# Optimization experiments

Hardware: AMD Instinct MI355X
Metric: run time of the kernel (lower is better)

Reference implementation:

```python
import jax, jax.numpy as jnp
import numpy as np

B, O, F = 64, 64, 1024
RN, RD = 16, 256
DEPTH = 2


def setup_inputs() -> dict:
    key = jax.random.key(0)
    ks = jax.random.split(key, 7)
    s_self = (2.0 / (F + F)) ** 0.5  # xavier-ish scale
    s_rel = (2.0 / (F + RD + F)) ** 0.5
    return {
        "x": jax.random.normal(ks[0], (B, O, F), jnp.float32),
        "A": jax.random.uniform(ks[1], (B, O, O * RN), jnp.float32),
        "R": jax.random.normal(ks[2], (RN, RD), jnp.float32),
        "Wself": jax.random.normal(ks[3], (DEPTH, F, F), jnp.float32) * s_self,
        "bself": jax.random.normal(ks[4], (DEPTH, F), jnp.float32) * 0.02,
        "Wrel": jax.random.normal(ks[5], (DEPTH, F + RD, F), jnp.float32) * s_rel,
        "brel": jax.random.normal(ks[6], (DEPTH, F), jnp.float32) * 0.02,
    }


def reference(x, A, R, Wself, bself, Wrel, brel):
    # x: [B,O,F], A: [B,O,O*RN], R: [RN,RD]
    b, o, f = x.shape
    rn = R.shape[0]
    depth = Wself.shape[0]
    for i in range(depth):
        # self transform: Linear(F -> F)
        xs = x @ Wself[i] + bself[i]  # [B,O,F]
        # relation transform: Linear(F+RD -> F) applied to concat(x_repeated, R_repeated).
        # Exact decomposition of the concat: first F rows of Wrel act on x, rest on R.
        xr_x = x @ Wrel[i][:f]                 # [B,O,F]
        xr_r = R @ Wrel[i][f:] + brel[i]       # [RN,F]
        xr = (xr_x[:, :, None, :] + xr_r[None, None, :, :]).reshape(b, o * rn, f)
        agg = jnp.matmul(A, xr)                # [B,O,F]
        x = jnp.tanh(xs + agg + x)             # residual + tanh
    return x
```

## Files before the change

### kernel.cpp

```cpp
#include <hip/hip_runtime.h>
#include <hip/hip_bf16.h>
#include <math.h>

#define B 64
#define O 64
#define F 1024
#define RN 16
#define RD 256
#define DEPTH 2
#define M (B*O)

typedef __attribute__((ext_vector_type(8))) _Float16 half8;
typedef __attribute__((ext_vector_type(4))) float f32x4;

#define RES_SCALE 2048.0f
#define RES_INV  (1.0f/2048.0f)

__device__ __forceinline__ unsigned short h2u(_Float16 h) {
  union { _Float16 h; unsigned short u; } c; c.h = h; return c.u;
}
__device__ __forceinline__ void split2(float x, unsigned short& h, unsigned short& l) {
  _Float16 hh = (_Float16)x;
  _Float16 ll = (_Float16)((x - (float)hh) * RES_SCALE);
  h = h2u(hh); l = h2u(ll);
}

__device__ __forceinline__ void gload_lds16(const unsigned short* g, void* l) {
  __builtin_amdgcn_global_load_lds(
      (const __attribute__((address_space(1))) unsigned int*)g,
      (__attribute__((address_space(3))) unsigned int*)l, 16, 0, 0);
}

__global__ __launch_bounds__(256) void k_reduceA(const float* __restrict__ A,
                                                 float* __restrict__ A1,
                                                 float* __restrict__ A2) {
  __shared__ float row[O * RN];
  const int bo = blockIdx.x;
  const int t = threadIdx.x;
  *reinterpret_cast<float4*>(&row[t * 4]) =
      *reinterpret_cast<const float4*>(&A[(size_t)bo * (O * RN) + t * 4]);
  __syncthreads();
  if (t < O) {
    float s = 0.f;
#pragma unroll
    for (int r = 0; r < RN; ++r) s += row[t * RN + r];
    A1[(size_t)bo * O + t] = s;
  } else if (t < O + RN) {
    const int r = t - O;
    float s = 0.f;
#pragma unroll
    for (int o2 = 0; o2 < O; ++o2) s += row[o2 * RN + r];
    A2[(size_t)bo * RN + r] = s;
  }
}

__global__ __launch_bounds__(256) void k_xrr(const float* __restrict__ R,
                                             const float* __restrict__ Wrel,
                                             const float* __restrict__ brel,
                                             float* __restrict__ xrr) {
  const int layer = blockIdx.y;
  const float* Wr = Wrel + (size_t)layer * (F + RD) * F + (size_t)F * F;
  const float* br = brel + (size_t)layer * F;
  const int r = blockIdx.x >> 2;
  const int n = ((blockIdx.x & 3) << 8) + threadIdx.x;
  float s = br[n];
  for (int k = 0; k < RD; ++k) s += R[r * RD + k] * Wr[(size_t)k * F + n];
  xrr[(size_t)layer * RN * F + (size_t)r * F + n] = s;
}

__global__ __launch_bounds__(256) void k_splitX(const float* __restrict__ X,
                                                unsigned short* __restrict__ Xh,
                                                unsigned short* __restrict__ Xl) {
  const size_t i = ((size_t)blockIdx.x * 256 + threadIdx.x) * 4;
  const float4 v = *reinterpret_cast<const float4*>(&X[i]);
  unsigned short h0, h1, h2, h3, l0, l1, l2, l3;
  split2(v.x, h0, l0); split2(v.y, h1, l1); split2(v.z, h2, l2); split2(v.w, h3, l3);
  uint2 hp, lp;
  hp.x = (unsigned)h0 | ((unsigned)h1 << 16); hp.y = (unsigned)h2 | ((unsigned)h3 << 16);
  lp.x = (unsigned)l0 | ((unsigned)l1 << 16); lp.y = (unsigned)l2 | ((unsigned)l3 << 16);
  *reinterpret_cast<uint2*>(&Xh[i]) = hp;
  *reinterpret_cast<uint2*>(&Xl[i]) = lp;
}

__global__ __launch_bounds__(256) void k_splitW2(const float* __restrict__ Wself,
                                                 const float* __restrict__ Wrel,
                                                 unsigned short* __restrict__ Wht,
                                                 unsigned short* __restrict__ Wlt) {
  __shared__ float T[32][33];
  const int layer = blockIdx.z >> 1;
  const int sel = blockIdx.z & 1;
  const float* W = sel ? (Wrel + (size_t)layer * (F + RD) * F)
                       : (Wself + (size_t)layer * F * F);
  const size_t obase = (size_t)layer * 2048 * 1024 + (size_t)(sel ? 1024 : 0) * 1024;
  const int k0 = blockIdx.x * 32, n0 = blockIdx.y * 32;
  const int t = threadIdx.x;
  const int r = t >> 3, c4 = (t & 7) << 2;
  const float4 v = *reinterpret_cast<const float4*>(&W[(size_t)(k0 + r) * 1024 + n0 + c4]);
  T[r][c4] = v.x; T[r][c4 + 1] = v.y; T[r][c4 + 2] = v.z; T[r][c4 + 3] = v.w;
  __syncthreads();
  unsigned short h[4], l[4];
#pragma unroll
  for (int j = 0; j < 4; ++j) split2(T[c4 + j][r], h[j], l[j]);
  uint2 hp, lp;
  hp.x = (unsigned)h[0] | ((unsigned)h[1] << 16); hp.y = (unsigned)h[2] | ((unsigned)h[3] << 16);
  lp.x = (unsigned)l[0] | ((unsigned)l[1] << 16); lp.y = (unsigned)l[2] | ((unsigned)l[3] << 16);
  const size_t o = obase + (size_t)(n0 + r) * 1024 + k0 + c4;
  *reinterpret_cast<uint2*>(&Wht[o]) = hp;
  *reinterpret_cast<uint2*>(&Wlt[o]) = lp;
}

__device__ __forceinline__ void stage_tiles8(const unsigned short* __restrict__ Asrc,
                                             const unsigned short* __restrict__ Bsrc,
                                             int bm, int bn, int k0,
                                             int w, int lane,
                                             char* Al, char* Bl) {
  const int srow = lane >> 3;
  const int sin = (lane & 7) << 4;
#pragma unroll
  for (int i = 0; i < 4; ++i) {
    const int c = (w << 2) + i;
    const int cc = c & 15;
    const int row = (cc << 3) + srow;
    const int inrow = sin ^ ((row & 7) << 4);
    const unsigned short* src = (c < 16) ? Asrc : Bsrc;
    const int rbase = (c < 16) ? bm : bn;
    char* ldst = (c < 16) ? Al : Bl;
    gload_lds16(src + ((size_t)(rbase + row) << 10) + k0 + (inrow >> 1), ldst + (cc << 10));
  }
}

__device__ __forceinline__ void compute_tile8(const char* Al, const char* Bl,
                                              int ar, int br, int kbyte,
                                              f32x4 (&acc)[4][2]) {
#pragma unroll
  for (int kk = 0; kk < 2; ++kk) {
    half8 a[4], b[2];
#pragma unroll
    for (int m = 0; m < 4; ++m) {
      const int row = ar + m * 16;
      const int off = (row << 7) + (((kk << 6) + kbyte) ^ ((row & 7) << 4));
      a[m] = *reinterpret_cast<const half8*>(&Al[off]);
    }
#pragma unroll
    for (int n = 0; n < 2; ++n) {
      const int row = br + n * 16;
      const int off = (row << 7) + (((kk << 6) + kbyte) ^ ((row & 7) << 4));
      b[n] = *reinterpret_cast<const half8*>(&Bl[off]);
    }
#pragma unroll
    for (int m = 0; m < 4; ++m)
#pragma unroll
      for (int n = 0; n < 2; ++n)
        acc[m][n] = __builtin_amdgcn_mfma_f32_16x16x32_f16(a[m], b[n], acc[m][n], 0, 0, 0);
  }
}

__device__ __forceinline__ void gemm_piece8(const unsigned short* __restrict__ Asrc,
                                            const unsigned short* __restrict__ Bsrc,
                                            int bm, int bn, int w, int lane,
                                            int ar, int br, int kbyte,
                                            char* Al, char* Bl, f32x4 (&acc)[4][2]) {
  for (int kt = 0; kt < 16; ++kt) {
    stage_tiles8(Asrc, Bsrc, bm, bn, kt << 6, w, lane, Al, Bl);
    __syncthreads();
    compute_tile8(Al, Bl, ar, br, kbyte, acc);
    __syncthreads();
  }
}

__global__ __launch_bounds__(512) void k_gemm_mfma(
    const unsigned short* __restrict__ Xh, const unsigned short* __restrict__ Xl,
    const unsigned short* __restrict__ Wht, const unsigned short* __restrict__ Wlt,
    float* __restrict__ xs, float* __restrict__ xrx, int xs_full) {
  __shared__ __align__(16) char Al[128 * 128];
  __shared__ __align__(16) char Bl[128 * 128];
  const int t = threadIdx.x;
  const int lane = t & 63, w = t >> 6;
  const int bid = blockIdx.x;
  const int half = bid & 1;
  int e = bid >> 1;
  e = (e & 7) * 32 + (e >> 3);
  const int bm = (e & 31) * 128;
  const int bn = (e >> 5) * 128 + (half ? 0 : 1024);
  const int wr = w >> 2, wc = w & 3;
  const bool full = (half == 0) || xs_full;

  f32x4 accM[4][2], accR[4][2];
#pragma unroll
  for (int m = 0; m < 4; ++m)
#pragma unroll
    for (int n = 0; n < 2; ++n) { accM[m][n] = (f32x4)0.f; accR[m][n] = (f32x4)0.f; }

  const int ar = wr * 64 + (lane & 15);
  const int br = wc * 32 + (lane & 15);
  const int kbyte = (lane >> 4) << 4;

  gemm_piece8(Xh, Wht, bm, bn, w, lane, ar, br, kbyte, Al, Bl, accM);
  if (full) {
    gemm_piece8(Xh, Wlt, bm, bn, w, lane, ar, br, kbyte, Al, Bl, accR);
    gemm_piece8(Xl, Wht, bm, bn, w, lane, ar, br, kbyte, Al, Bl, accR);
  }

  float* dst = (bn < 1024) ? xs : xrx;
  const int coff = bn & 1023;
  const int lrow = (lane >> 4) << 2;
  const int lcol = lane & 15;
#pragma unroll
  for (int m = 0; m < 4; ++m)
#pragma unroll
    for (int n = 0; n < 2; ++n) {
      const int gr = bm + wr * 64 + m * 16 + lrow;
      const int gc = coff + wc * 32 + n * 16 + lcol;
#pragma unroll
      for (int i = 0; i < 4; ++i)
        dst[((size_t)(gr + i) << 10) + gc] = accM[m][n][i] + accR[m][n][i] * RES_INV;
    }
}

__global__ __launch_bounds__(256) void k_agg(const float* __restrict__ A1,
                                             const float* __restrict__ A2,
                                             const float* __restrict__ xrx,
                                             const float* __restrict__ xrr,
                                             const float* __restrict__ xs,
                                             const float* __restrict__ bias,
                                             const float* __restrict__ xin,
                                             float* __restrict__ xout,
                                             unsigned short* __restrict__ XhO,
                                             unsigned short* __restrict__ XlO) {
  __shared__ float A1s[O][O + 1];
  __shared__ float A2s[O][RN + 1];
  __shared__ float Xls[O][132];
  __shared__ float Rls[RN][132];
  const int b = blockIdx.x;
  const int f0 = blockIdx.y * 128;
  const int t = threadIdx.x;

#pragma unroll
  for (int i = 0; i < 4; ++i) {
    const int gi = i * 1024 + t * 4;
    const float4 v = *reinterpret_cast<const float4*>(&A1[(size_t)b * O * O + gi]);
    const int o = gi >> 6, c = gi & 63;
    A1s[o][c] = v.x; A1s[o][c + 1] = v.y; A1s[o][c + 2] = v.z; A1s[o][c + 3] = v.w;
  }
  {
    const int gi = t * 4;
    const float4 v = *reinterpret_cast<const float4*>(&A2[(size_t)b * O * RN + gi]);
    const int o = gi >> 4, c = gi & 15;
    A2s[o][c] = v.x; A2s[o][c + 1] = v.y; A2s[o][c + 2] = v.z; A2s[o][c + 3] = v.w;
  }
#pragma unroll
  for (int i = 0; i < 8; ++i) {
    const int gi = i * 1024 + t * 4;
    const int o2 = gi >> 7, c = gi & 127;
    const float4 v = *reinterpret_cast<const float4*>(&xrx[((size_t)(b * O + o2)) * F + f0 + c]);
    Xls[o2][c] = v.x; Xls[o2][c + 1] = v.y; Xls[o2][c + 2] = v.z; Xls[o2][c + 3] = v.w;
  }
#pragma unroll
  for (int i = 0; i < 2; ++i) {
    const int gi = i * 1024 + t * 4;
    const int r = gi >> 7, c = gi & 127;
    const float4 v = *reinterpret_cast<const float4*>(&xrr[(size_t)r * F + f0 + c]);
    Rls[r][c] = v.x; Rls[r][c + 1] = v.y; Rls[r][c + 2] = v.z; Rls[r][c + 3] = v.w;
  }
  __syncthreads();

  const int ob = (t >> 4) << 2;
  const int fc = (t & 15) << 2;
  float acc[4][8];
#pragma unroll
  for (int i = 0; i < 4; ++i)
#pragma unroll
    for (int j = 0; j < 8; ++j) acc[i][j] = 0.f;

#pragma unroll 4
  for (int o2 = 0; o2 < O; ++o2) {
    const float4 xa = *reinterpret_cast<const float4*>(&Xls[o2][fc]);
    const float4 xb = *reinterpret_cast<const float4*>(&Xls[o2][fc + 64]);
#pragma unroll
    for (int io = 0; io < 4; ++io) {
      const float a = A1s[ob + io][o2];
      acc[io][0] += a * xa.x; acc[io][1] += a * xa.y; acc[io][2] += a * xa.z; acc[io][3] += a * xa.w;
      acc[io][4] += a * xb.x; acc[io][5] += a * xb.y; acc[io][6] += a * xb.z; acc[io][7] += a * xb.w;
    }
  }
#pragma unroll
  for (int r = 0; r < RN; ++r) {
    const float4 xa = *reinterpret_cast<const float4*>(&Rls[r][fc]);
    const float4 xb = *reinterpret_cast<const float4*>(&Rls[r][fc + 64]);
#pragma unroll
    for (int io = 0; io < 4; ++io) {
      const float a = A2s[ob + io][r];
      acc[io][0] += a * xa.x; acc[io][1] += a * xa.y; acc[io][2] += a * xa.z; acc[io][3] += a * xa.w;
      acc[io][4] += a * xb.x; acc[io][5] += a * xb.y; acc[io][6] += a * xb.z; acc[io][7] += a * xb.w;
    }
  }

#pragma unroll
  for (int io = 0; io < 4; ++io) {
    const size_t base = ((size_t)(b * O + ob + io)) * F + f0;
#pragma unroll
    for (int seg = 0; seg < 2; ++seg) {
      const size_t idx = base + seg * 64 + fc;
      const float4 s = *reinterpret_cast<const float4*>(&xs[idx]);
      const float4 bv = *reinterpret_cast<const float4*>(&bias[f0 + seg * 64 + fc]);
      const float4 xi = *reinterpret_cast<const float4*>(&xin[idx]);
      float4 o;
      o.x = tanhf(acc[io][seg * 4 + 0] + s.x + bv.x + xi.x);
      o.y = tanhf(acc[io][seg * 4 + 1] + s.y + bv.y + xi.y);
      o.z = tanhf(acc[io][seg * 4 + 2] + s.z + bv.z + xi.z);
      o.w = tanhf(acc[io][seg * 4 + 3] + s.w + bv.w + xi.w);
      *reinterpret_cast<float4*>(&xout[idx]) = o;
      if (XhO) {
        unsigned short h0, h1, h2, h3, l0, l1, l2, l3;
        split2(o.x, h0, l0); split2(o.y, h1, l1); split2(o.z, h2, l2); split2(o.w, h3, l3);
        uint2 hp, lp;
        hp.x = (unsigned)h0 | ((unsigned)h1 << 16); hp.y = (unsigned)h2 | ((unsigned)h3 << 16);
        lp.x = (unsigned)l0 | ((unsigned)l1 << 16); lp.y = (unsigned)l2 | ((unsigned)l3 << 16);
        *reinterpret_cast<uint2*>(&XhO[idx]) = hp;
        *reinterpret_cast<uint2*>(&XlO[idx]) = lp;
      }
    }
  }
}

extern "C" void kernel_launch(void* const* d_in, const int* in_sizes, int n_in,
                              void* d_out, int out_size, void* d_ws, size_t ws_size,
                              hipStream_t stream) {
  const float* x0    = (const float*)d_in[0];
  const float* A     = (const float*)d_in[1];
  const float* R     = (const float*)d_in[2];
  const float* Wself = (const float*)d_in[3];
  const float* bself = (const float*)d_in[4];
  const float* Wrel  = (const float*)d_in[5];
  const float* brel  = (const float*)d_in[6];
  float* out = (float*)d_out;

  float* ws  = (float*)d_ws;
  float* A1  = ws;
  float* A2  = A1 + (size_t)M * O;
  float* xrr = A2 + (size_t)M * RN;
  float* xs  = xrr + (size_t)2 * RN * F;
  float* xrx = xs + (size_t)M * F;
  unsigned short* Xh  = (unsigned short*)(xrx + (size_t)M * F);
  unsigned short* Xl  = Xh + (size_t)M * F;
  unsigned short* Wht = Xl + (size_t)M * F;
  unsigned short* Wlt = Wht + (size_t)2 * 2048 * 1024;

  k_reduceA<<<M, 256, 0, stream>>>(A, A1, A2);
  k_splitX<<<4096, 256, 0, stream>>>(x0, Xh, Xl);
  k_splitW2<<<dim3(32, 32, 4), 256, 0, stream>>>(Wself, Wrel, Wht, Wlt);
  k_xrr<<<dim3(RN * 4, 2), 256, 0, stream>>>(R, Wrel, brel, xrr);

  for (int i = 0; i < DEPTH; ++i) {
    const float* X = (i == 0) ? x0 : out;
    const unsigned short* Wht_i = Wht + (size_t)i * 2048 * 1024;
    const unsigned short* Wlt_i = Wlt + (size_t)i * 2048 * 1024;
    const int xs_full = (i + 1 < DEPTH) ? 1 : 0;
    k_gemm_mfma<<<512, 512, 0, stream>>>(Xh, Xl, Wht_i, Wlt_i, xs, xrx, xs_full);
    const bool emit = (i + 1 < DEPTH);
    k_agg<<<dim3(B, F / 128), 256, 0, stream>>>(A1, A2, xrx,
                                                xrr + (size_t)i * RN * F, xs,
                                                bself + (size_t)i * F, X, out,
                                                emit ? Xh : nullptr,
                                                emit ? Xl : nullptr);
  }
}
```

Measured before the change: 183.3 us.

## Merge prep kernels and split layer-2 GEMM residual terms across more blocks

Merges the four preprocessing kernels into two launches by dispatching on block index. The second-layer GEMM becomes a new kernel with 1024 blocks, each computing one of four products (xs high, xrx high, and two residual-correction partials) into separate buffers. The aggregation kernel then sums those partials. This doubles parallelism for the final GEMM and cuts launch count, at the cost of extra partial-buffer traffic and a different xs accuracy path in layer 2.

```diff
diff --git a/kernel.cpp b/kernel.cpp
--- a/kernel.cpp
+++ b/kernel.cpp
@@ -31,82 +31,88 @@
       (__attribute__((address_space(3))) unsigned int*)l, 16, 0, 0);
 }
 
-__global__ __launch_bounds__(256) void k_reduceA(const float* __restrict__ A,
-                                                 float* __restrict__ A1,
-                                                 float* __restrict__ A2) {
+__global__ __launch_bounds__(256) void k_prep(const float* __restrict__ A,
+                                              const float* __restrict__ X,
+                                              float* __restrict__ A1,
+                                              float* __restrict__ A2,
+                                              unsigned short* __restrict__ Xh,
+                                              unsigned short* __restrict__ Xl) {
   __shared__ float row[O * RN];
-  const int bo = blockIdx.x;
   const int t = threadIdx.x;
-  *reinterpret_cast<float4*>(&row[t * 4]) =
-      *reinterpret_cast<const float4*>(&A[(size_t)bo * (O * RN) + t * 4]);
-  __syncthreads();
-  if (t < O) {
-    float s = 0.f;
-#pragma unroll
-    for (int r = 0; r < RN; ++r) s += row[t * RN + r];
-    A1[(size_t)bo * O + t] = s;
-  } else if (t < O + RN) {
-    const int r = t - O;
-    float s = 0.f;
-#pragma unroll
-    for (int o2 = 0; o2 < O; ++o2) s += row[o2 * RN + r];
-    A2[(size_t)bo * RN + r] = s;
-  }
-}
-
-__global__ __launch_bounds__(256) void k_xrr(const float* __restrict__ R,
-                                             const float* __restrict__ Wrel,
-                                             const float* __restrict__ brel,
-                                             float* __restrict__ xrr) {
-  const int layer = blockIdx.y;
-  const float* Wr = Wrel + (size_t)layer * (F + RD) * F + (size_t)F * F;
-  const float* br = brel + (size_t)layer * F;
-  const int r = blockIdx.x >> 2;
-  const int n = ((blockIdx.x & 3) << 8) + threadIdx.x;
-  float s = br[n];
-  for (int k = 0; k < RD; ++k) s += R[r * RD + k] * Wr[(size_t)k * F + n];
-  xrr[(size_t)layer * RN * F + (size_t)r * F + n] = s;
-}
-
-__global__ __launch_bounds__(256) void k_splitX(const float* __restrict__ X,
-                                                unsigned short* __restrict__ Xh,
-                                                unsigned short* __restrict__ Xl) {
-  const size_t i = ((size_t)blockIdx.x * 256 + threadIdx.x) * 4;
-  const float4 v = *reinterpret_cast<const float4*>(&X[i]);
-  unsigned short h0, h1, h2, h3, l0, l1, l2, l3;
-  split2(v.x, h0, l0); split2(v.y, h1, l1); split2(v.z, h2, l2); split2(v.w, h3, l3);
-  uint2 hp, lp;
-  hp.x = (unsigned)h0 | ((unsigned)h1 << 16); hp.y = (unsigned)h2 | ((unsigned)h3 << 16);
-  lp.x = (unsigned)l0 | ((unsigned)l1 << 16); lp.y = (unsigned)l2 | ((unsigned)l3 << 16);
-  *reinterpret_cast<uint2*>(&Xh[i]) = hp;
-  *reinterpret_cast<uint2*>(&Xl[i]) = lp;
-}
-
-__global__ __launch_bounds__(256) void k_splitW2(const float* __restrict__ Wself,
-                                                 const float* __restrict__ Wrel,
-                                                 unsigned short* __restrict__ Wht,
-                                                 unsigned short* __restrict__ Wlt) {
+  if (blockIdx.x < 4096) {
+    const int bo = blockIdx.x;
+    *reinterpret_cast<float4*>(&row[t * 4]) =
+        *reinterpret_cast<const float4*>(&A[(size_t)bo * (O * RN) + t * 4]);
+    __syncthreads();
+    if (t < O) {
+      float s = 0.f;
+#pragma unroll
+      for (int r = 0; r < RN; ++r) s += row[t * RN + r];
+      A1[(size_t)bo * O + t] = s;
+    } else if (t < O + RN) {
+      const int r = t - O;
+      float s = 0.f;
+#pragma unroll
+      for (int o2 = 0; o2 < O; ++o2) s += row[o2 * RN + r];
+      A2[(size_t)bo * RN + r] = s;
+    }
+  } else {
+    const size_t i = ((size_t)(blockIdx.x - 4096) * 256 + t) * 4;
+    const float4 v = *reinterpret_cast<const float4*>(&X[i]);
+    unsigned short h0, h1, h2, h3, l0, l1, l2, l3;
+    split2(v.x, h0, l0); split2(v.y, h1, l1); split2(v.z, h2, l2); split2(v.w, h3, l3);
+    uint2 hp, lp;
+    hp.x = (unsigned)h0 | ((unsigned)h1 << 16); hp.y = (unsigned)h2 | ((unsigned)h3 << 16);
+    lp.x = (unsigned)l0 | ((unsigned)l1 << 16); lp.y = (unsigned)l2 | ((unsigned)l3 << 16);
+    *reinterpret_cast<uint2*>(&Xh[i]) = hp;
+    *reinterpret_cast<uint2*>(&Xl[i]) = lp;
+  }
+}
+
+__global__ __launch_bounds__(256) void k_prepW(const float* __restrict__ Wself,
+                                               const float* __restrict__ Wrel,
+                                               const float* __restrict__ brel,
+                                               const float* __restrict__ R,
+                                               unsigned short* __restrict__ Wht,
+                                               unsigned short* __restrict__ Wlt,
+                                               float* __restrict__ xrr) {
   __shared__ float T[32][33];
-  const int layer = blockIdx.z >> 1;
-  const int sel = blockIdx.z & 1;
-  const float* W = sel ? (Wrel + (size_t)layer * (F + RD) * F)
-                       : (Wself + (size_t)layer * F * F);
-  const size_t obase = (size_t)layer * 2048 * 1024 + (size_t)(sel ? 1024 : 0) * 1024;
-  const int k0 = blockIdx.x * 32, n0 = blockIdx.y * 32;
   const int t = threadIdx.x;
-  const int r = t >> 3, c4 = (t & 7) << 2;
-  const float4 v = *reinterpret_cast<const float4*>(&W[(size_t)(k0 + r) * 1024 + n0 + c4]);
-  T[r][c4] = v.x; T[r][c4 + 1] = v.y; T[r][c4 + 2] = v.z; T[r][c4 + 3] = v.w;
-  __syncthreads();
-  unsigned short h[4], l[4];
-#pragma unroll
-  for (int j = 0; j < 4; ++j) split2(T[c4 + j][r], h[j], l[j]);
-  uint2 hp, lp;
-  hp.x = (unsigned)h[0] | ((unsigned)h[1] << 16); hp.y = (unsigned)h[2] | ((unsigned)h[3] << 16);
-  lp.x = (unsigned)l[0] | ((unsigned)l[1] << 16); lp.y = (unsigned)l[2] | ((unsigned)l[3] << 16);
-  const size_t o = obase + (size_t)(n0 + r) * 1024 + k0 + c4;
-  *reinterpret_cast<uint2*>(&Wht[o]) = hp;
-  *reinterpret_cast<uint2*>(&Wlt[o]) = lp;
+  const int bid = blockIdx.x;
+  if (bid < 4096) {
+    const int z = bid >> 10;
+    const int rem = bid & 1023;
+    const int k0 = (rem & 31) * 32, n0 = (rem >> 5) * 32;
+    const int layer = z >> 1;
+    const int sel = z & 1;
+    const float* W = sel ? (Wrel + (size_t)layer * (F + RD) * F)
+                         : (Wself + (size_t)layer * F * F);
+    const size_t obase = (size_t)layer * 2048 * 1024 + (size_t)(sel ? 1024 : 0) * 1024;
+    const int r = t >> 3, c4 = (t & 7) << 2;
+    const float4 v = *reinterpret_cast<const float4*>(&W[(size_t)(k0 + r) * 1024 + n0 + c4]);
+    T[r][c4] = v.x; T[r][c4 + 1] = v.y; T[r][c4 + 2] = v.z; T[r][c4 + 3] = v.w;
+    __syncthreads();
+    unsigned short h[4], l[4];
+#pragma unroll
+    for (int j = 0; j < 4; ++j) split2(T[c4 + j][r], h[j], l[j]);
+    uint2 hp, lp;
+    hp.x = (unsigned)h[0] | ((unsigned)h[1] << 16); hp.y = (unsigned)h[2] | ((unsigned)h[3] << 16);
+    lp.x = (unsigned)l[0] | ((unsigned)l[1] << 16); lp.y = (unsigned)l[2] | ((unsigned)l[3] << 16);
+    const size_t o = obase + (size_t)(n0 + r) * 1024 + k0 + c4;
+    *reinterpret_cast<uint2*>(&Wht[o]) = hp;
+    *reinterpret_cast<uint2*>(&Wlt[o]) = lp;
+  } else {
+    const int r4 = bid - 4096;
+    const int layer = r4 >> 6;
+    const int idx = r4 & 63;
+    const float* Wr = Wrel + (size_t)layer * (F + RD) * F + (size_t)F * F;
+    const float* br = brel + (size_t)layer * F;
+    const int r = idx >> 2;
+    const int n = ((idx & 3) << 8) + t;
+    float s = br[n];
+    for (int k = 0; k < RD; ++k) s += R[r * RD + k] * Wr[(size_t)k * F + n];
+    xrr[(size_t)layer * RN * F + (size_t)r * F + n] = s;
+  }
 }
 
 __device__ __forceinline__ void stage_tiles8(const unsigned short* __restrict__ Asrc,
@@ -217,16 +223,66 @@
     }
 }
 
+__global__ __launch_bounds__(512) void k_gemm_l2(
+    const unsigned short* __restrict__ Xh, const unsigned short* __restrict__ Xl,
+    const unsigned short* __restrict__ Wht, const unsigned short* __restrict__ Wlt,
+    float* __restrict__ xs, float* __restrict__ xrx,
+    float* __restrict__ P1, float* __restrict__ P2) {
+  __shared__ __align__(16) char Al[128 * 128];
+  __shared__ __align__(16) char Bl[128 * 128];
+  const int t = threadIdx.x;
+  const int lane = t & 63, w = t >> 6;
+  const int bid = blockIdx.x;
+  const int role = bid & 3;
+  int e = bid >> 2;
+  e = (e & 7) * 32 + (e >> 3);
+  const int bm = (e & 31) * 128;
+  const int colblk = (e >> 5) * 128;
+  const int bn = (role == 0) ? colblk : 1024 + colblk;
+  const unsigned short* Asrc = (role == 3) ? Xl : Xh;
+  const unsigned short* Bsrc = (role == 2) ? Wlt : Wht;
+  float* dst = (role == 0) ? xs : (role == 1) ? xrx : (role == 2) ? P1 : P2;
+  const int wr = w >> 2, wc = w & 3;
+
+  f32x4 acc[4][2];
+#pragma unroll
+  for (int m = 0; m < 4; ++m)
+#pragma unroll
+    for (int n = 0; n < 2; ++n) acc[m][n] = (f32x4)0.f;
+
+  const int ar = wr * 64 + (lane & 15);
+  const int br = wc * 32 + (lane & 15);
+  const int kbyte = (lane >> 4) << 4;
+
+  gemm_piece8(Asrc, Bsrc, bm, bn, w, lane, ar, br, kbyte, Al, Bl, acc);
+
+  const int lrow = (lane >> 4) << 2;
+  const int lcol = lane & 15;
+#pragma unroll
+  for (int m = 0; m < 4; ++m)
+#pragma unroll
+    for (int n = 0; n < 2; ++n) {
+      const int gr = bm + wr * 64 + m * 16 + lrow;
+      const int gc = colblk + wc * 32 + n * 16 + lcol;
+#pragma unroll
+      for (int i = 0; i < 4; ++i)
+        dst[((size_t)(gr + i) << 10) + gc] = acc[m][n][i];
+    }
+}
+
 __global__ __launch_bounds__(256) void k_agg(const float* __restrict__ A1,
                                              const float* __restrict__ A2,
                                              const float* __restrict__ xrx,
+                                             const float* __restrict__ P1,
+                                             const float* __restrict__ P2,
                                              const float* __restrict__ xrr,
                                              const float* __restrict__ xs,
                                              const float* __restrict__ bias,
                                              const float* __restrict__ xin,
                                              float* __restrict__ xout,
                                              unsigned short* __restrict__ XhO,
-                                             unsigned short* __restrict__ XlO) {
+                                             unsigned short* __restrict__ XlO,
+                                             int use_p) {
   __shared__ float A1s[O][O + 1];
   __shared__ float A2s[O][RN + 1];
   __shared__ float Xls[O][132];
@@ -252,7 +308,14 @@
   for (int i = 0; i < 8; ++i) {
     const int gi = i * 1024 + t * 4;
     const int o2 = gi >> 7, c = gi & 127;
-    const float4 v = *reinterpret_cast<const float4*>(&xrx[((size_t)(b * O + o2)) * F + f0 + c]);
+    const size_t pidx = ((size_t)(b * O + o2)) * F + f0 + c;
+    float4 v = *reinterpret_cast<const float4*>(&xrx[pidx]);
+    if (use_p) {
+      const float4 p1 = *reinterpret_cast<const float4*>(&P1[pidx]);
+      const float4 p2 = *reinterpret_cast<const float4*>(&P2[pidx]);
+      v.x += (p1.x + p2.x) * RES_INV; v.y += (p1.y + p2.y) * RES_INV;
+      v.z += (p1.z + p2.z) * RES_INV; v.w += (p1.w + p2.w) * RES_INV;
+    }
     Xls[o2][c] = v.x; Xls[o2][c + 1] = v.y; Xls[o2][c + 2] = v.z; Xls[o2][c + 3] = v.w;
   }
 #pragma unroll
@@ -341,27 +404,26 @@
   float* xrr = A2 + (size_t)M * RN;
   float* xs  = xrr + (size_t)2 * RN * F;
   float* xrx = xs + (size_t)M * F;
-  unsigned short* Xh  = (unsigned short*)(xrx + (size_t)M * F);
+  float* P1  = xrx + (size_t)M * F;
+  float* P2  = P1 + (size_t)M * F;
+  unsigned short* Xh  = (unsigned short*)(P2 + (size_t)M * F);
   unsigned short* Xl  = Xh + (size_t)M * F;
   unsigned short* Wht = Xl + (size_t)M * F;
   unsigned short* Wlt = Wht + (size_t)2 * 2048 * 1024;
 
-  k_reduceA<<<M, 256, 0, stream>>>(A, A1, A2);
-  k_splitX<<<4096, 256, 0, stream>>>(x0, Xh, Xl);
-  k_splitW2<<<dim3(32, 32, 4), 256, 0, stream>>>(Wself, Wrel, Wht, Wlt);
-  k_xrr<<<dim3(RN * 4, 2), 256, 0, stream>>>(R, Wrel, brel, xrr);
-
-  for (int i = 0; i < DEPTH; ++i) {
-    const float* X = (i == 0) ? x0 : out;
-    const unsigned short* Wht_i = Wht + (size_t)i * 2048 * 1024;
-    const unsigned short* Wlt_i = Wlt + (size_t)i * 2048 * 1024;
-    const int xs_full = (i + 1 < DEPTH) ? 1 : 0;
-    k_gemm_mfma<<<512, 512, 0, stream>>>(Xh, Xl, Wht_i, Wlt_i, xs, xrx, xs_full);
-    const bool emit = (i + 1 < DEPTH);
-    k_agg<<<dim3(B, F / 128), 256, 0, stream>>>(A1, A2, xrx,
-                                                xrr + (size_t)i * RN * F, xs,
-                                                bself + (size_t)i * F, X, out,
-                                                emit ? Xh : nullptr,
-                                                emit ? Xl : nullptr);
-  }
-}
+  k_prep<<<8192, 256, 0, stream>>>(A, x0, A1, A2, Xh, Xl);
+  k_prepW<<<4096 + 128, 256, 0, stream>>>(Wself, Wrel, brel, R, Wht, Wlt, xrr);
+
+  k_gemm_mfma<<<512, 512, 0, stream>>>(Xh, Xl, Wht, Wlt, xs, xrx, 1);
+  k_agg<<<dim3(B, F / 128), 256, 0, stream>>>(A1, A2, xrx, P1, P2,
+                                              xrr, xs, bself, x0, out,
+                                              Xh, Xl, 0);
+  k_gemm_l2<<<1024, 512, 0, stream>>>(Xh, Xl,
+                                      Wht + (size_t)2048 * 1024,
+                                      Wlt + (size_t)2048 * 1024,
+                                      xs, xrx, P1, P2);
+  k_agg<<<dim3(B, F / 128), 256, 0, stream>>>(A1, A2, xrx, P1, P2,
+                                              xrr + (size_t)RN * F, xs,
+                                              bself + (size_t)F, out, out,
+                                              nullptr, nullptr, 1);
+}
```

New measurement: 169.9 us. 1.08x faster.
